# Kernel optimization log

Hardware: AMD Instinct MI355X
Metric: run time of the kernel (lower is better)

The kernel has to match this reference:

```python
import jax, jax.numpy as jnp
import numpy as np

NUM_MOVABLE = 4096
NUM_PHYS = 4096
NOTCH_THRESH = 2.0


def setup_inputs() -> dict:
    key = jax.random.key(0)
    k1, k2, k3 = jax.random.split(key, 3)
    # positions spread over a chip-scale region so gaps are a mix of open/violating
    pos = jax.random.normal(k1, (2 * NUM_PHYS,), dtype=jnp.float32) * 50.0
    macro_mask = jnp.ones((NUM_MOVABLE,), dtype=bool)  # all movable nodes are macros
    macro_size_x = jax.random.uniform(k2, (NUM_MOVABLE,), dtype=jnp.float32) * 4.0 + 1.0
    macro_size_y = jax.random.uniform(k3, (NUM_MOVABLE,), dtype=jnp.float32) * 4.0 + 1.0
    return {"pos": pos, "macro_mask": macro_mask,
            "macro_size_x": macro_size_x, "macro_size_y": macro_size_y}


def reference(pos, macro_mask, macro_size_x, macro_size_y):
    # macro_mask is all-True by construction, so the boolean gather
    # pos[:num_movable][macro_mask] is a static slice (jit-compatible).
    x = pos[:NUM_MOVABLE]                                  # [N]
    y = pos[NUM_PHYS:NUM_PHYS + NUM_MOVABLE]               # [N]
    N = x.shape[0]
    sx = macro_size_x.astype(x.dtype)
    sy = macro_size_y.astype(x.dtype)

    cx_diff = jnp.abs(x[:, None] - x[None, :])             # [N,N]
    cy_diff = jnp.abs(y[:, None] - y[None, :])             # [N,N]
    half_w = (sx[:, None] + sx[None, :]) * 0.5             # [N,N]
    half_h = (sy[:, None] + sy[None, :]) * 0.5             # [N,N]

    dx_gap = jax.nn.relu(cx_diff - half_w)
    dy_gap = jax.nn.relu(cy_diff - half_h)
    d_ij = dx_gap + dy_gap                                 # edge-to-edge L1 gap

    penalty = jax.nn.relu(NOTCH_THRESH - d_ij)             # [N,N]
    ut_mask = jnp.triu(jnp.ones((N, N), dtype=bool), 1)    # strict upper triangle
    # torch: relu(thresh - d_ij[ut_mask]).pow(2).sum() == masked sum of squares
    return jnp.sum(jnp.where(ut_mask, penalty * penalty, jnp.zeros((), x.dtype)))
```

## Files before the change

kernel.cpp:

```cpp
#include <hip/hip_runtime.h>

#define N 4096
#define ROWS_PER_BLOCK 16
#define NBLOCKS (N / ROWS_PER_BLOCK)
#define THREADS 512
#define R 4
#define CCHUNKS (THREADS / R)
#define JPT (N / CCHUNKS)
#define NOTCH_THRESH 2.0f

__global__ __launch_bounds__(THREADS) void notch_main(
    const float* __restrict__ pos,
    const float* __restrict__ sx,
    const float* __restrict__ sy,
    float* __restrict__ partial)
{
    __shared__ float4 tile[N];
    __shared__ float red[THREADS / 64];

    const int tid = threadIdx.x;

    for (int j = tid; j < N; j += THREADS) {
        float4 t;
        t.x = pos[j];
        t.y = pos[N + j];
        t.z = 0.5f * sx[j];
        t.w = 0.5f * sy[j];
        tile[j] = t;
    }
    __syncthreads();

    const int g  = tid & (R - 1);
    const int c  = tid >> 2;
    const int i0 = blockIdx.x * ROWS_PER_BLOCK + g * R;

    const float4 me0 = tile[i0 + 0];
    const float4 me1 = tile[i0 + 1];
    const float4 me2 = tile[i0 + 2];
    const float4 me3 = tile[i0 + 3];

    float a0 = 0.0f, a1 = 0.0f, a2 = 0.0f, a3 = 0.0f;

#define PAIR(me, acc) {                                      \
        float dx = fabsf(me.x - t.x) - (me.z + t.z);         \
        float dy = fabsf(me.y - t.y) - (me.w + t.w);         \
        float d  = fmaxf(dx, 0.0f) + fmaxf(dy, 0.0f);        \
        float p  = fmaxf(NOTCH_THRESH - d, 0.0f);            \
        acc = fmaf(p, p, acc); }

    #pragma unroll 4
    for (int jj = 0; jj < JPT; ++jj) {
        const float4 t = tile[jj * CCHUNKS + c];
        PAIR(me0, a0)
        PAIR(me1, a1)
        PAIR(me2, a2)
        PAIR(me3, a3)
    }
#undef PAIR

    float acc = (a0 + a1) + (a2 + a3);

    for (int off = 32; off > 0; off >>= 1)
        acc += __shfl_down(acc, off, 64);
    const int wave = tid >> 6;
    const int lane = tid & 63;
    if (lane == 0) red[wave] = acc;
    __syncthreads();
    if (tid == 0) {
        float s = 0.0f;
        #pragma unroll
        for (int w = 0; w < THREADS / 64; ++w) s += red[w];
        partial[blockIdx.x] = s;
    }
}

__global__ __launch_bounds__(256) void notch_final(
    const float* __restrict__ partial, float* __restrict__ out)
{
    __shared__ float red[4];
    const int tid = threadIdx.x;
    float v = partial[tid];
    for (int off = 32; off > 0; off >>= 1)
        v += __shfl_down(v, off, 64);
    if ((tid & 63) == 0) red[tid >> 6] = v;
    __syncthreads();
    if (tid == 0) {
        const float total = red[0] + red[1] + red[2] + red[3];
        out[0] = (total - 4.0f * (float)N) * 0.5f;
    }
}

extern "C" void kernel_launch(void* const* d_in, const int* in_sizes, int n_in,
                              void* d_out, int out_size, void* d_ws, size_t ws_size,
                              hipStream_t stream) {
    const float* pos = (const float*)d_in[0];
    const float* sx  = (const float*)d_in[2];
    const float* sy  = (const float*)d_in[3];
    float* out     = (float*)d_out;
    float* partial = (float*)d_ws;

    notch_main<<<NBLOCKS, THREADS, 0, stream>>>(pos, sx, sy, partial);
    notch_final<<<1, 256, 0, stream>>>(partial, out);
}
```

Measured before the change: 65.11 us.

## Fuse final reduction via last-block atomic counter and precompute box edges

Merges the two-kernel reduction into one kernel: each block publishes its partial sum, bumps an atomic counter, and the last block to arrive reduces all partials and writes the output. The shared tile now stores box min/max edges instead of center and half-size, so each pair's gap becomes a max of two subtractions, saving an abs and an add per axis. This trades a second kernel launch for a memset launch plus atomic and fence traffic.

```diff
diff --git a/kernel.cpp b/kernel.cpp
--- a/kernel.cpp
+++ b/kernel.cpp
@@ -9,23 +9,30 @@
 #define JPT (N / CCHUNKS)
 #define NOTCH_THRESH 2.0f
 
-__global__ __launch_bounds__(THREADS) void notch_main(
+__global__ __launch_bounds__(THREADS) void notch_fused(
     const float* __restrict__ pos,
     const float* __restrict__ sx,
     const float* __restrict__ sy,
-    float* __restrict__ partial)
+    float* __restrict__ partial,
+    unsigned int* __restrict__ counter,
+    float* __restrict__ out)
 {
     __shared__ float4 tile[N];
     __shared__ float red[THREADS / 64];
+    __shared__ int is_last;
 
     const int tid = threadIdx.x;
 
     for (int j = tid; j < N; j += THREADS) {
+        const float x  = pos[j];
+        const float y  = pos[N + j];
+        const float hx = 0.5f * sx[j];
+        const float hy = 0.5f * sy[j];
         float4 t;
-        t.x = pos[j];
-        t.y = pos[N + j];
-        t.z = 0.5f * sx[j];
-        t.w = 0.5f * sy[j];
+        t.x = x - hx;
+        t.y = x + hx;
+        t.z = y - hy;
+        t.w = y + hy;
         tile[j] = t;
     }
     __syncthreads();
@@ -41,11 +48,10 @@
 
     float a0 = 0.0f, a1 = 0.0f, a2 = 0.0f, a3 = 0.0f;
 
-#define PAIR(me, acc) {                                      \
-        float dx = fabsf(me.x - t.x) - (me.z + t.z);         \
-        float dy = fabsf(me.y - t.y) - (me.w + t.w);         \
-        float d  = fmaxf(dx, 0.0f) + fmaxf(dy, 0.0f);        \
-        float p  = fmaxf(NOTCH_THRESH - d, 0.0f);            \
+#define PAIR(me, acc) {                                              \
+        float dxp = fmaxf(fmaxf(me.x - t.y, t.x - me.y), 0.0f);      \
+        float dyp = fmaxf(fmaxf(me.z - t.w, t.z - me.w), 0.0f);      \
+        float p   = fmaxf(NOTCH_THRESH - (dxp + dyp), 0.0f);         \
         acc = fmaf(p, p, acc); }
 
     #pragma unroll 4
@@ -66,27 +72,35 @@
     const int lane = tid & 63;
     if (lane == 0) red[wave] = acc;
     __syncthreads();
+
     if (tid == 0) {
         float s = 0.0f;
         #pragma unroll
         for (int w = 0; w < THREADS / 64; ++w) s += red[w];
-        partial[blockIdx.x] = s;
+        __hip_atomic_store(&partial[blockIdx.x], s, __ATOMIC_RELEASE,
+                           __HIP_MEMORY_SCOPE_AGENT);
+        const unsigned int old = __hip_atomic_fetch_add(
+            counter, 1u, __ATOMIC_ACQ_REL, __HIP_MEMORY_SCOPE_AGENT);
+        is_last = (old == NBLOCKS - 1);
     }
-}
+    __syncthreads();
 
-__global__ __launch_bounds__(256) void notch_final(
-    const float* __restrict__ partial, float* __restrict__ out)
-{
-    __shared__ float red[4];
-    const int tid = threadIdx.x;
-    float v = partial[tid];
-    for (int off = 32; off > 0; off >>= 1)
-        v += __shfl_down(v, off, 64);
-    if ((tid & 63) == 0) red[tid >> 6] = v;
-    __syncthreads();
-    if (tid == 0) {
-        const float total = red[0] + red[1] + red[2] + red[3];
-        out[0] = (total - 4.0f * (float)N) * 0.5f;
+    if (is_last) {
+        __shared__ float red2[NBLOCKS / 64];
+        if (tid < NBLOCKS) {
+            float v = __hip_atomic_load(&partial[tid], __ATOMIC_RELAXED,
+                                        __HIP_MEMORY_SCOPE_AGENT);
+            for (int off = 32; off > 0; off >>= 1)
+                v += __shfl_down(v, off, 64);
+            if ((tid & 63) == 0) red2[tid >> 6] = v;
+        }
+        __syncthreads();
+        if (tid == 0) {
+            float total = 0.0f;
+            #pragma unroll
+            for (int w = 0; w < NBLOCKS / 64; ++w) total += red2[w];
+            out[0] = (total - 4.0f * (float)N) * 0.5f;
+        }
     }
 }
 
@@ -96,9 +110,12 @@
     const float* pos = (const float*)d_in[0];
     const float* sx  = (const float*)d_in[2];
     const float* sy  = (const float*)d_in[3];
-    float* out     = (float*)d_out;
-    float* partial = (float*)d_ws;
+    float* out = (float*)d_out;
 
-    notch_main<<<NBLOCKS, THREADS, 0, stream>>>(pos, sx, sy, partial);
-    notch_final<<<1, 256, 0, stream>>>(partial, out);
+    unsigned int* counter = (unsigned int*)d_ws;
+    float* partial = (float*)((char*)d_ws + 256);
+
+    hipMemsetAsync(counter, 0, sizeof(unsigned int), stream);
+
+    notch_fused<<<NBLOCKS, THREADS, 0, stream>>>(pos, sx, sy, partial, counter, out);
 }
```

Measured after the change: 73.53 us. 1.13x slower.
